# Kernel optimization log

Hardware: AMD Instinct MI355X
Metric: run time of the kernel (lower is better)

Reference implementation:

```python
import jax, jax.numpy as jnp
import numpy as np

NUM_GROUPS = 2048  # ix values drawn from [0, NUM_GROUPS); stands in for torch.unique's group count

def setup_inputs() -> dict:
    key = jax.random.key(0)
    ks = jax.random.split(key, 9)
    B, E, D = 2, 32768, 512
    s = 1.0 / np.sqrt(D)  # nn.Linear default init scale
    x = jax.random.normal(ks[0], (B, E, D), jnp.float32)
    ix = jax.random.randint(ks[1], (E,), 0, NUM_GROUPS)
    Wf = jax.random.uniform(ks[2], (D, D), jnp.float32, -s, s)
    bf = jax.random.uniform(ks[3], (D,), jnp.float32, -s, s)
    Wg = jax.random.uniform(ks[4], (D, D), jnp.float32, -s, s)
    bg = jax.random.uniform(ks[5], (D,), jnp.float32, -s, s)
    Wh = jax.random.uniform(ks[6], (D, D), jnp.float32, -s, s)
    bh = jax.random.uniform(ks[7], (D,), jnp.float32, -s, s)
    return {"x": x, "ix": ix, "Wf": Wf, "bf": bf, "Wg": Wg, "bg": bg, "Wh": Wh, "bh": bh}

def reference(x, ix, Wf, bf, Wg, bg, Wh, bh):
    # Linear projections (nn.Linear: x @ W.T + b)
    logits = jnp.einsum('bed,kd->bek', x, Wg) + bg  # g(x): (B,E,D)
    vals   = jnp.einsum('bed,kd->bek', x, Wf) + bf  # f(x): (B,E,D)
    # Move edges to leading axis for segment ops: (E,B,D)
    lt = jnp.transpose(logits, (1, 0, 2))
    vt = jnp.transpose(vals, (1, 0, 2))
    # Group-wise (scatter) softmax over edges sharing the same ix
    m = jax.ops.segment_max(lt, ix, num_segments=NUM_GROUPS)      # (G,B,D)
    e = jnp.exp(lt - m[ix])                                        # (E,B,D)
    denom = jax.ops.segment_sum(e, ix, num_segments=NUM_GROUPS)   # (G,B,D)
    w = e / denom[ix]                                              # (E,B,D)
    # Weighted scatter-sum per group
    y = jax.ops.segment_sum(vt * w, ix, num_segments=NUM_GROUPS)  # (G,B,D)
    y = jnp.transpose(y, (1, 0, 2))                                # (B,G,D)
    out = jnp.einsum('bgd,kd->bgk', y, Wh) + bh                    # h(y)
    return out[:, ix]                                              # expand back to (B,E,D)
```

## Files before the change

kernel.cpp:

```cpp
#include <hip/hip_runtime.h>
#include <hip/hip_bf16.h>
#include <cstdint>
#include <cstddef>

typedef __bf16 bf16x8 __attribute__((ext_vector_type(8)));
typedef float f32x4 __attribute__((ext_vector_type(4)));
using u16 = unsigned short;

#define NUM_GROUPS_C 2048

__device__ __forceinline__ u16 f2bf(float f) {
  union { float f; uint32_t u; } c; c.f = f;
  uint32_t r = (c.u + 0x7fffu + ((c.u >> 16) & 1u)) >> 16;
  return (u16)r;
}
__device__ __forceinline__ float bf2f(u16 h) {
  union { uint32_t u; float f; } c; c.u = ((uint32_t)h) << 16; return c.f;
}

__device__ __forceinline__ void glds16(const u16* g, void* l) {
  __builtin_amdgcn_global_load_lds((const __attribute__((address_space(1))) void*)g,
                                   (__attribute__((address_space(3))) void*)l, 16, 0, 0);
}

__global__ void cast_f32_bf16(const float* __restrict__ src, u16* __restrict__ dst, long n4) {
  long i = (long)blockIdx.x * blockDim.x + threadIdx.x;
  long stride = (long)gridDim.x * blockDim.x;
  for (; i < n4; i += stride) {
    float4 v = reinterpret_cast<const float4*>(src)[i];
    uint2 o;
    o.x = (uint32_t)f2bf(v.x) | ((uint32_t)f2bf(v.y) << 16);
    o.y = (uint32_t)f2bf(v.z) | ((uint32_t)f2bf(v.w) << 16);
    reinterpret_cast<uint2*>(dst)[i] = o;
  }
}

__global__ void cast_w3(const float* __restrict__ w0, const float* __restrict__ w1,
                        const float* __restrict__ w2,
                        u16* __restrict__ o0, u16* __restrict__ o1, u16* __restrict__ o2,
                        int n4) {
  const float* src = (blockIdx.y == 0) ? w0 : (blockIdx.y == 1) ? w1 : w2;
  u16* dst = (blockIdx.y == 0) ? o0 : (blockIdx.y == 1) ? o1 : o2;
  int i = blockIdx.x * blockDim.x + threadIdx.x;
  int stride = gridDim.x * blockDim.x;
  for (; i < n4; i += stride) {
    float4 v = reinterpret_cast<const float4*>(src)[i];
    uint2 o;
    o.x = (uint32_t)f2bf(v.x) | ((uint32_t)f2bf(v.y) << 16);
    o.y = (uint32_t)f2bf(v.z) | ((uint32_t)f2bf(v.w) << 16);
    reinterpret_cast<uint2*>(dst)[i] = o;
  }
}

__global__ void zero_i32(int* p, int n) {
  int i = blockIdx.x * blockDim.x + threadIdx.x;
  if (i < n) p[i] = 0;
}
__global__ void count_k(const int* __restrict__ ix, int* __restrict__ cnt, int E) {
  int e = blockIdx.x * blockDim.x + threadIdx.x;
  if (e < E) atomicAdd(&cnt[ix[e]], 1);
}
__global__ void scan_k(const int* __restrict__ cnt, int* __restrict__ offs,
                       int* __restrict__ cursor, int G) {
  __shared__ int part[256];
  int t = threadIdx.x;
  int gpt = G / 256;
  int base = t * gpt;
  int loc[8];
  int s = 0;
  for (int j = 0; j < gpt; ++j) { loc[j] = cnt[base + j]; s += loc[j]; }
  part[t] = s;
  __syncthreads();
  for (int off = 1; off < 256; off <<= 1) {
    int v = (t >= off) ? part[t - off] : 0;
    __syncthreads();
    part[t] += v;
    __syncthreads();
  }
  int run = part[t] - s;
  for (int j = 0; j < gpt; ++j) {
    offs[base + j] = run;
    cursor[base + j] = run;
    run += loc[j];
  }
}
__global__ void scatter_k(const int* __restrict__ ix, int* __restrict__ cursor,
                          int* __restrict__ elist, int E) {
  int e = blockIdx.x * blockDim.x + threadIdx.x;
  if (e < E) {
    int g = ix[e];
    int pos = atomicAdd(&cursor[g], 1);
    elist[pos] = e;
  }
}

__global__ __launch_bounds__(512, 2)
void gemm256_fg8(const u16* __restrict__ A,
                 const u16* __restrict__ B0g, const u16* __restrict__ B1g,
                 const float* __restrict__ bias0, const float* __restrict__ bias1,
                 u16* __restrict__ C0, u16* __restrict__ C1,
                 int K, int N) {
  __shared__ u16 lds[65536];

  const int tid  = threadIdx.x;
  const int lane = tid & 63;
  const int wid  = tid >> 6;
  const int wm   = wid >> 2;
  const int wn   = wid & 3;
  const int fr   = lane & 15;
  const int fq   = lane >> 4;
  const int swr  = fr & 7;

  const int nwg = gridDim.x, cpx = nwg >> 3, wg = blockIdx.x;
  const int swz = (wg & 7) * cpx + (wg >> 3);
  const int mt = swz >> 2, ns = swz & 3;
  const u16* Bm     = (ns < 2) ? B0g : B1g;
  const float* bias = (ns < 2) ? bias0 : bias1;
  u16* C            = (ns < 2) ? C0 : C1;
  const int n0 = (ns & 1) * 256, m0 = mt * 256;

  const int r8   = tid >> 3;
  const int scol = ((tid & 7) ^ (r8 & 7)) << 3;
  const u16* Ab = A  + (size_t)m0 * K + scol;
  const u16* Bb = Bm + (size_t)n0 * K + scol;
  char* ldsb = (char*)lds;

  auto stage_ht = [&](int p, int isB, int h, int kt) {
    const u16* src = (isB ? Bb : Ab) + (size_t)(h * 128 + r8) * K + kt * 64;
    char* dst = ldsb + p * 65536 + isB * 32768 + h * 16384 + wid * 1024;
    glds16(src, dst);
    glds16(src + (size_t)64 * K, dst + 8192);
  };

#define RD_A(dst, mi_, kk_) \
  dst = *(const bf16x8*)(sA_ + (((mi_) * 32 + wm * 16 + fr) << 7) + (((((kk_) << 2) | fq) ^ swr) << 4))
#define RD_B(dst, nj_, kk_) \
  dst = *(const bf16x8*)(sB_ + (((nj_) * 64 + wn * 16 + fr) << 7) + (((((kk_) << 2) | fq) ^ swr) << 4))
#define MFMA_Q(accm, accn, af, bf_)                                                \
  __builtin_amdgcn_s_setprio(1);                                                  \
  _Pragma("unroll") for (int j = 0; j < 4; ++j)                                    \
  _Pragma("unroll") for (int jn = 0; jn < 2; ++jn)                                 \
  _Pragma("unroll") for (int kk = 0; kk < 2; ++kk)                                 \
    acc[(accm) + j][(accn) + jn] = __builtin_amdgcn_mfma_f32_16x16x32_bf16(        \
        af[j][kk], bf_[jn][kk], acc[(accm) + j][(accn) + jn], 0, 0, 0);            \
  __builtin_amdgcn_s_setprio(0);

  f32x4 acc[8][4] = {};
  const int NT = K >> 6;

  stage_ht(0, 1, 0, 0);
  stage_ht(0, 0, 0, 0);
  stage_ht(0, 1, 1, 0);
  stage_ht(0, 0, 1, 0);
  asm volatile("s_waitcnt vmcnt(4)" ::: "memory");
  __builtin_amdgcn_s_barrier();

  for (int kt = 0; kt < NT; ++kt) {
    const int cb = kt & 1, nb = cb ^ 1;
    const int ks = (kt + 1 < NT) ? kt + 1 : NT - 1;
    const char* sA_ = ldsb + cb * 65536;
    const char* sB_ = sA_ + 32768;
    bf16x8 a0[4][2], a1[4][2], b0[2][2], b1[2][2];

    #pragma unroll
    for (int j = 0; j < 4; ++j) { RD_A(a0[j][0], j, 0); RD_A(a0[j][1], j, 1); }
    #pragma unroll
    for (int j = 0; j < 2; ++j) { RD_B(b0[j][0], j, 0); RD_B(b0[j][1], j, 1); }
    stage_ht(nb, 1, 0, ks);
    asm volatile("s_waitcnt vmcnt(4)" ::: "memory");
    __builtin_amdgcn_s_barrier();
    MFMA_Q(0, 0, a0, b0)
    __builtin_amdgcn_s_barrier();

    #pragma unroll
    for (int j = 0; j < 2; ++j) { RD_B(b1[j][0], j + 2, 0); RD_B(b1[j][1], j + 2, 1); }
    stage_ht(nb, 0, 0, ks);
    asm volatile("s_waitcnt vmcnt(4)" ::: "memory");
    __builtin_amdgcn_s_barrier();
    MFMA_Q(0, 2, a0, b1)
    __builtin_amdgcn_s_barrier();

    #pragma unroll
    for (int j = 0; j < 4; ++j) { RD_A(a1[j][0], j + 4, 0); RD_A(a1[j][1], j + 4, 1); }
    stage_ht(nb, 1, 1, ks);
    asm volatile("s_waitcnt vmcnt(4)" ::: "memory");
    __builtin_amdgcn_s_barrier();
    MFMA_Q(4, 2, a1, b1)
    __builtin_amdgcn_s_barrier();

    stage_ht(nb, 0, 1, ks);
    asm volatile("s_waitcnt vmcnt(4)" ::: "memory");
    __builtin_amdgcn_s_barrier();
    MFMA_Q(4, 0, a1, b0)
    __builtin_amdgcn_s_barrier();
  }
  asm volatile("s_waitcnt vmcnt(0)" ::: "memory");

  #pragma unroll
  for (int mi = 0; mi < 8; ++mi) {
    const int row = m0 + mi * 32 + wm * 16 + fq * 4;
    #pragma unroll
    for (int ni = 0; ni < 4; ++ni) {
      const int col = n0 + ni * 64 + wn * 16 + fr;
      const float bvv = bias[col];
      #pragma unroll
      for (int r = 0; r < 4; ++r)
        C[(size_t)(row + r) * N + col] = f2bf(acc[mi][ni][r] + bvv);
    }
  }
#undef RD_A
#undef RD_B
#undef MFMA_Q
}

__device__ __forceinline__ void stage_tile_128x64(const u16* __restrict__ src, int ld,
                                                  u16* lds, int tid) {
  int wid = tid >> 6;
  #pragma unroll
  for (int i = 0; i < 4; ++i) {
    int c = i * 256 + tid;
    const u16* g = src + (size_t)(c >> 3) * ld + ((c & 7) << 3);
    char* l = (char*)lds + ((i * 4 + wid) << 10);
    glds16(g, l);
  }
}

__global__ __launch_bounds__(256)
void gemm_bf16_nt_f32out(const u16* __restrict__ A, const u16* __restrict__ Bm,
                         const float* __restrict__ bias,
                         float* __restrict__ C, int K, int N) {
  __shared__ u16 sA[128 * 64];
  __shared__ u16 sB[128 * 64];

  int tid = threadIdx.x;
  const int m0 = blockIdx.x * 128, n0 = blockIdx.y * 128;
  const u16* Ap = A + (size_t)m0 * K;
  const u16* Bp = Bm + (size_t)n0 * K;

  int lane = tid & 63;
  int wid = tid >> 6;
  int wm = wid >> 1, wn = wid & 1;
  int fr = lane & 15;
  int fq = lane >> 4;

  f32x4 acc[4][4] = {};

  for (int k0 = 0; k0 < K; k0 += 64) {
    stage_tile_128x64(Ap + k0, K, sA, tid);
    stage_tile_128x64(Bp + k0, K, sB, tid);
    __syncthreads();
    #pragma unroll
    for (int kk = 0; kk < 2; ++kk) {
      bf16x8 af[4], bfrag[4];
      #pragma unroll
      for (int mi = 0; mi < 4; ++mi)
        af[mi] = *reinterpret_cast<const bf16x8*>(&sA[(wm * 64 + mi * 16 + fr) * 64 + kk * 32 + fq * 8]);
      #pragma unroll
      for (int nj = 0; nj < 4; ++nj)
        bfrag[nj] = *reinterpret_cast<const bf16x8*>(&sB[(wn * 64 + nj * 16 + fr) * 64 + kk * 32 + fq * 8]);
      #pragma unroll
      for (int mi = 0; mi < 4; ++mi)
        #pragma unroll
        for (int nj = 0; nj < 4; ++nj)
          acc[mi][nj] = __builtin_amdgcn_mfma_f32_16x16x32_bf16(af[mi], bfrag[nj], acc[mi][nj], 0, 0, 0);
    }
    __syncthreads();
  }

  #pragma unroll
  for (int nj = 0; nj < 4; ++nj) {
    int col = n0 + wn * 64 + nj * 16 + fr;
    float bv = bias[col];
    #pragma unroll
    for (int mi = 0; mi < 4; ++mi) {
      int rowb = m0 + wm * 64 + mi * 16 + fq * 4;
      #pragma unroll
      for (int r = 0; r < 4; ++r)
        C[(size_t)(rowb + r) * N + col] = acc[mi][nj][r] + bv;
    }
  }
}

__global__ __launch_bounds__(256)
void seg_softmax(const u16* __restrict__ lg, const u16* __restrict__ vl,
                 const int* __restrict__ cnt, const int* __restrict__ offs,
                 const int* __restrict__ elist,
                 u16* __restrict__ y, int E, int D, int B, int G) {
  __shared__ int eids[256];
  int g = blockIdx.x / B;
  int b = blockIdx.x - g * B;
  int t = threadIdx.x;
  int n = cnt[g], start = offs[g];
  int d0 = t * 2;

  float m0 = -1e30f, m1 = -1e30f, s0 = 0.f, s1 = 0.f, a0 = 0.f, a1 = 0.f;
  for (int c0 = 0; c0 < n; c0 += 256) {
    int nc = n - c0; if (nc > 256) nc = 256;
    __syncthreads();
    if (t < nc) eids[t] = elist[start + c0 + t];
    __syncthreads();
    for (int i = 0; i < nc; ++i) {
      size_t base = ((size_t)b * E + eids[i]) * D + d0;
      uint32_t lu = *reinterpret_cast<const uint32_t*>(lg + base);
      uint32_t vu = *reinterpret_cast<const uint32_t*>(vl + base);
      float l0 = bf2f((u16)(lu & 0xffffu)), l1 = bf2f((u16)(lu >> 16));
      float v0 = bf2f((u16)(vu & 0xffffu)), v1 = bf2f((u16)(vu >> 16));
      float nm0 = fmaxf(m0, l0);
      float sc0 = __expf(m0 - nm0), w0 = __expf(l0 - nm0);
      s0 = s0 * sc0 + w0; a0 = a0 * sc0 + w0 * v0; m0 = nm0;
      float nm1 = fmaxf(m1, l1);
      float sc1 = __expf(m1 - nm1), w1 = __expf(l1 - nm1);
      s1 = s1 * sc1 + w1; a1 = a1 * sc1 + w1 * v1; m1 = nm1;
    }
  }
  float r0 = (n > 0) ? a0 / s0 : 0.f;
  float r1 = (n > 0) ? a1 / s1 : 0.f;
  size_t yoff = ((size_t)b * G + g) * D + d0;
  uint32_t o = (uint32_t)f2bf(r0) | ((uint32_t)f2bf(r1) << 16);
  *reinterpret_cast<uint32_t*>(y + yoff) = o;
}

__global__ void gather_k(const float* __restrict__ of, const int* __restrict__ ix,
                         float* __restrict__ out, int E, int D, int G) {
  int be = blockIdx.x;
  int b = be / E;
  int e = be - b * E;
  int gsel = ix[e];
  const float4* src = reinterpret_cast<const float4*>(of + ((size_t)b * G + gsel) * D);
  float4* dst = reinterpret_cast<float4*>(out + (size_t)be * D);
  for (int t = threadIdx.x; t < D / 4; t += blockDim.x)
    dst[t] = src[t];
}

extern "C" void kernel_launch(void* const* d_in, const int* in_sizes, int n_in,
                              void* d_out, int out_size, void* d_ws, size_t ws_size,
                              hipStream_t stream) {
  const float* x   = (const float*)d_in[0];
  const int*   ix  = (const int*)d_in[1];
  const float* Wf  = (const float*)d_in[2];
  const float* bfb = (const float*)d_in[3];
  const float* Wg  = (const float*)d_in[4];
  const float* bg  = (const float*)d_in[5];
  const float* Wh  = (const float*)d_in[6];
  const float* bh  = (const float*)d_in[7];

  const int E = in_sizes[1];
  const int D = in_sizes[3];
  const int B = in_sizes[0] / (E * D);
  const int G = NUM_GROUPS_C;
  const int M = B * E;
  const long xn = (long)M * D;

  char* ws = (char*)d_ws;
  size_t off = 0;
  auto alloc = [&](size_t bytes) -> char* {
    char* p = ws + off;
    off += (bytes + 255) & ~(size_t)255;
    return p;
  };
  u16* xb  = (u16*)alloc((size_t)M * D * 2);
  u16* lgb = (u16*)alloc((size_t)M * D * 2);
  u16* vlb = (u16*)alloc((size_t)M * D * 2);
  u16* Wgb = (u16*)alloc((size_t)D * D * 2);
  u16* Wfb = (u16*)alloc((size_t)D * D * 2);
  u16* Whb = (u16*)alloc((size_t)D * D * 2);
  u16* yb  = (u16*)alloc((size_t)B * G * D * 2);
  float* ofb = (float*)alloc((size_t)B * G * D * 4);
  int* cnt    = (int*)alloc((size_t)G * 4);
  int* offs   = (int*)alloc((size_t)G * 4);
  int* cursor = (int*)alloc((size_t)G * 4);
  int* elist  = (int*)alloc((size_t)E * 4);

  cast_f32_bf16<<<2048, 256, 0, stream>>>(x, xb, xn / 4);
  dim3 gw(64, 3);
  cast_w3<<<gw, 256, 0, stream>>>(Wg, Wf, Wh, Wgb, Wfb, Whb, D * D / 4);

  zero_i32<<<(G + 255) / 256, 256, 0, stream>>>(cnt, G);
  count_k<<<(E + 255) / 256, 256, 0, stream>>>(ix, cnt, E);
  scan_k<<<1, 256, 0, stream>>>(cnt, offs, cursor, G);
  scatter_k<<<(E + 255) / 256, 256, 0, stream>>>(ix, cursor, elist, E);

  gemm256_fg8<<<(M / 256) * 4, 512, 0, stream>>>(xb, Wgb, Wfb, bg, bfb, lgb, vlb, D, D);

  seg_softmax<<<G * B, 256, 0, stream>>>(lgb, vlb, cnt, offs, elist, yb, E, D, B, G);

  dim3 gh((B * G) / 128, D / 128);
  gemm_bf16_nt_f32out<<<gh, 256, 0, stream>>>(yb, Whb, bh, ofb, D, D);

  gather_k<<<B * E, 128, 0, stream>>>(ofb, ix, (float*)d_out, E, D, G);
}
```

Baseline: 222.0 us.

## Software-pipeline LDS fragment reads with MFMA in the fused f/g GEMM

Restructures the main loop of the fused logits/values GEMM so the LDS reads for the next quarter-tile, including the next k-tile's A fragments, are issued while the current MFMA quarter runs. It also drops the barrier pairs that used to surround each MFMA group. The k-loop is unrolled by two so the double-buffer index is a compile-time constant. This aims to hide LDS read latency and cut barrier stalls in the compute-bound GEMM, at the cost of more live registers and tighter reasoning about buffer-reuse hazards, since fewer barriers guard the overwritten buffer. The loop assumes NT is even, which holds for K=512.

```diff
diff --git a/kernel.cpp b/kernel.cpp
--- a/kernel.cpp
+++ b/kernel.cpp
@@ -95,11 +95,11 @@
 }
 
 __global__ __launch_bounds__(512, 2)
-void gemm256_fg8(const u16* __restrict__ A,
-                 const u16* __restrict__ B0g, const u16* __restrict__ B1g,
-                 const float* __restrict__ bias0, const float* __restrict__ bias1,
-                 u16* __restrict__ C0, u16* __restrict__ C1,
-                 int K, int N) {
+void gemm256_pl(const u16* __restrict__ A,
+                const u16* __restrict__ B0g, const u16* __restrict__ B1g,
+                const float* __restrict__ bias0, const float* __restrict__ bias1,
+                u16* __restrict__ C0, u16* __restrict__ C1,
+                int K, int N) {
   __shared__ u16 lds[65536];
 
   const int tid  = threadIdx.x;
@@ -132,10 +132,16 @@
     glds16(src + (size_t)64 * K, dst + 8192);
   };
 
-#define RD_A(dst, mi_, kk_) \
-  dst = *(const bf16x8*)(sA_ + (((mi_) * 32 + wm * 16 + fr) << 7) + (((((kk_) << 2) | fq) ^ swr) << 4))
-#define RD_B(dst, nj_, kk_) \
-  dst = *(const bf16x8*)(sB_ + (((nj_) * 64 + wn * 16 + fr) << 7) + (((((kk_) << 2) | fq) ^ swr) << 4))
+#define RD4_A(dst, base, mio)                                                       \
+  _Pragma("unroll") for (int j = 0; j < 4; ++j)                                     \
+  _Pragma("unroll") for (int kk = 0; kk < 2; ++kk)                                  \
+    dst[j][kk] = *(const bf16x8*)((base) + ((((mio) + j) * 32 + wm * 16 + fr) << 7) \
+                                         + ((((kk << 2) | fq) ^ swr) << 4));
+#define RD2_B(dst, base, njo)                                                       \
+  _Pragma("unroll") for (int j = 0; j < 2; ++j)                                     \
+  _Pragma("unroll") for (int kk = 0; kk < 2; ++kk)                                  \
+    dst[j][kk] = *(const bf16x8*)((base) + ((((njo) + j) * 64 + wn * 16 + fr) << 7) \
+                                         + ((((kk << 2) | fq) ^ swr) << 4));
 #define MFMA_Q(accm, accn, af, bf_)                                                \
   __builtin_amdgcn_s_setprio(1);                                                  \
   _Pragma("unroll") for (int j = 0; j < 4; ++j)                                    \
@@ -146,55 +152,59 @@
   __builtin_amdgcn_s_setprio(0);
 
   f32x4 acc[8][4] = {};
+  bf16x8 a0[4][2], a1[4][2], b0[2][2], b1[2][2];
   const int NT = K >> 6;
 
   stage_ht(0, 1, 0, 0);
   stage_ht(0, 0, 0, 0);
   stage_ht(0, 1, 1, 0);
   stage_ht(0, 0, 1, 0);
-  asm volatile("s_waitcnt vmcnt(4)" ::: "memory");
+  asm volatile("s_waitcnt vmcnt(0)" ::: "memory");
   __builtin_amdgcn_s_barrier();
-
-  for (int kt = 0; kt < NT; ++kt) {
-    const int cb = kt & 1, nb = cb ^ 1;
-    const int ks = (kt + 1 < NT) ? kt + 1 : NT - 1;
-    const char* sA_ = ldsb + cb * 65536;
-    const char* sB_ = sA_ + 32768;
-    bf16x8 a0[4][2], a1[4][2], b0[2][2], b1[2][2];
-
-    #pragma unroll
-    for (int j = 0; j < 4; ++j) { RD_A(a0[j][0], j, 0); RD_A(a0[j][1], j, 1); }
-    #pragma unroll
-    for (int j = 0; j < 2; ++j) { RD_B(b0[j][0], j, 0); RD_B(b0[j][1], j, 1); }
-    stage_ht(nb, 1, 0, ks);
-    asm volatile("s_waitcnt vmcnt(4)" ::: "memory");
-    __builtin_amdgcn_s_barrier();
-    MFMA_Q(0, 0, a0, b0)
-    __builtin_amdgcn_s_barrier();
-
-    #pragma unroll
-    for (int j = 0; j < 2; ++j) { RD_B(b1[j][0], j + 2, 0); RD_B(b1[j][1], j + 2, 1); }
-    stage_ht(nb, 0, 0, ks);
-    asm volatile("s_waitcnt vmcnt(4)" ::: "memory");
-    __builtin_amdgcn_s_barrier();
-    MFMA_Q(0, 2, a0, b1)
-    __builtin_amdgcn_s_barrier();
-
-    #pragma unroll
-    for (int j = 0; j < 4; ++j) { RD_A(a1[j][0], j + 4, 0); RD_A(a1[j][1], j + 4, 1); }
-    stage_ht(nb, 1, 1, ks);
-    asm volatile("s_waitcnt vmcnt(4)" ::: "memory");
-    __builtin_amdgcn_s_barrier();
-    MFMA_Q(4, 2, a1, b1)
-    __builtin_amdgcn_s_barrier();
-
-    stage_ht(nb, 0, 1, ks);
-    asm volatile("s_waitcnt vmcnt(4)" ::: "memory");
-    __builtin_amdgcn_s_barrier();
-    MFMA_Q(4, 0, a1, b0)
-    __builtin_amdgcn_s_barrier();
+  RD4_A(a0, ldsb, 0)
+
+#define KT_BODY(cb_, kt_)                                                          \
+  {                                                                                \
+    const int nb_ = (cb_) ^ 1;                                                     \
+    const int ks_ = ((kt_) + 1 < NT) ? (kt_) + 1 : NT - 1;                         \
+    const char* sA_ = ldsb + (cb_) * 65536;                                        \
+    const char* sB_ = sA_ + 32768;                                                 \
+    const char* nA_ = ldsb + nb_ * 65536;                                          \
+                                                                          \
+    RD2_B(b0, sB_, 0)                                                              \
+    RD2_B(b1, sB_, 2)                                                              \
+    MFMA_Q(0, 0, a0, b0)                                                           \
+    stage_ht(nb_, 1, 0, ks_);                                                      \
+    asm volatile("s_waitcnt vmcnt(2)" ::: "memory");                               \
+    __builtin_amdgcn_s_barrier();                                                  \
+                                                                          \
+    RD4_A(a1, sA_, 4)                                                              \
+    MFMA_Q(0, 2, a0, b1)                                                           \
+    stage_ht(nb_, 0, 0, ks_);                                                      \
+    __builtin_amdgcn_s_barrier();                                                  \
+                                                                          \
+    MFMA_Q(4, 2, a1, b1)                                                           \
+    stage_ht(nb_, 1, 1, ks_);                                                      \
+    asm volatile("s_waitcnt vmcnt(2)" ::: "memory");                               \
+    __builtin_amdgcn_s_barrier();                                                  \
+           \
+    RD4_A(a0, nA_, 0)                                                              \
+    MFMA_Q(4, 0, a1, b0)                                                           \
+    stage_ht(nb_, 0, 1, ks_);                                                      \
+    asm volatile("s_waitcnt vmcnt(2)" ::: "memory");                               \
+    __builtin_amdgcn_s_barrier();                                                  \
+  }
+
+  for (int kt = 0; kt < NT; kt += 2) {
+    KT_BODY(0, kt)
+    KT_BODY(1, kt + 1)
   }
   asm volatile("s_waitcnt vmcnt(0)" ::: "memory");
+
+#undef KT_BODY
+#undef RD4_A
+#undef RD2_B
+#undef MFMA_Q
 
   #pragma unroll
   for (int mi = 0; mi < 8; ++mi) {
@@ -208,9 +218,6 @@
         C[(size_t)(row + r) * N + col] = f2bf(acc[mi][ni][r] + bvv);
     }
   }
-#undef RD_A
-#undef RD_B
-#undef MFMA_Q
 }
 
 __device__ __forceinline__ void stage_tile_128x64(const u16* __restrict__ src, int ld,
@@ -380,7 +387,7 @@
   scan_k<<<1, 256, 0, stream>>>(cnt, offs, cursor, G);
   scatter_k<<<(E + 255) / 256, 256, 0, stream>>>(ix, cursor, elist, E);
 
-  gemm256_fg8<<<(M / 256) * 4, 512, 0, stream>>>(xb, Wgb, Wfb, bg, bfb, lgb, vlb, D, D);
+  gemm256_pl<<<(M / 256) * 4, 512, 0, stream>>>(xb, Wgb, Wfb, bg, bfb, lgb, vlb, D, D);
 
   seg_softmax<<<G * B, 256, 0, stream>>>(lgb, vlb, cnt, offs, elist, yb, E, D, B, G);
 
```

Measured after the change: 225.9 us. About the same (+1.8%).
